# Optimization experiments

Hardware: AMD Instinct MI355X
Metric: run time of the kernel (lower is better)

Reference implementation:

```python
import jax, jax.numpy as jnp
import numpy as np

B, N, FEAT, HID = 1024, 128, 512, 256


def setup_inputs() -> dict:
    key = jax.random.key(0)
    k1, k2, k3, k4, k5, k6 = jax.random.split(key, 6)
    x = jax.random.normal(k1, (B, FEAT), dtype=jnp.float32)
    labels = jax.random.randint(k2, (B,), 0, N, dtype=jnp.int64)
    W_proj = jax.random.normal(k3, (FEAT, HID), dtype=jnp.float32) / np.sqrt(FEAT)
    b_proj = jax.random.normal(k4, (HID,), dtype=jnp.float32) * 0.01
    means = jax.random.normal(k5, (N, HID), dtype=jnp.float32)
    # inverse covariances must be SPD so sqrt(dist_sq) is real
    A = jax.random.normal(k6, (N, HID, HID), dtype=jnp.float32)
    inv_covs = jnp.einsum('nij,nkj->nik', A, A) / HID + 0.1 * jnp.eye(HID, dtype=jnp.float32)
    return {"x": x, "labels": labels, "W_proj": W_proj, "b_proj": b_proj,
            "means": means, "inv_covs": inv_covs}


def reference(x, labels, W_proj, b_proj, means, inv_covs):
    b = x.shape[0]
    n = means.shape[0]
    x_proj = x @ W_proj + b_proj                       # (b, hid)
    delta = x_proj[:, None, :] - means[None, :, :]     # (b, n, hid)
    # batched Mahalanobis quadratic form
    dist_sq = jnp.einsum('bni,nij,bnj->bn', delta, inv_covs, delta)
    distmat = jnp.sqrt(dist_sq + 1e-12)                # (b, n)
    center_mask = (labels[:, None] == jnp.arange(n)[None, :]).astype(distmat.dtype)
    loss = jnp.clip(distmat * center_mask, 1e-12, 1e12).sum() / b
    return loss, distmat
```

## Files before the change

kernel.cpp:

```cpp
#include <hip/hip_runtime.h>
#include <hip/hip_bf16.h>

#define B_    1024
#define N_    128
#define FEAT_ 512
#define HID_  256
#define LDK   264

typedef __bf16 bf16x8 __attribute__((ext_vector_type(8)));
typedef float  f32x4  __attribute__((ext_vector_type(4)));

__device__ __forceinline__ unsigned int f2bf(float f) {
    unsigned int u = __float_as_uint(f);
    u += 0x7fffu + ((u >> 16) & 1u);
    return u >> 16;
}
__device__ __forceinline__ unsigned int pack2(float a, float b) {
    return f2bf(a) | (f2bf(b) << 16);
}

union U16x8 { uint4 u; bf16x8 v; };

__global__ __launch_bounds__(256) void proj_kernel(
    const float* __restrict__ x, const float* __restrict__ W,
    const float* __restrict__ bias, float* __restrict__ xp)
{
    const int h  = threadIdx.x;
    const int b0 = blockIdx.x * 2;
    const float bb = bias[h];
    float a0 = bb, a1 = bb;
    const float* x0p = x + (size_t)(b0 + 0) * FEAT_;
    const float* x1p = x + (size_t)(b0 + 1) * FEAT_;
    #pragma unroll 4
    for (int f = 0; f < FEAT_; f += 4) {
        const float4 xv0 = *(const float4*)(x0p + f);
        const float4 xv1 = *(const float4*)(x1p + f);
        const float w0 = W[(size_t)(f + 0) * HID_ + h];
        const float w1 = W[(size_t)(f + 1) * HID_ + h];
        const float w2 = W[(size_t)(f + 2) * HID_ + h];
        const float w3 = W[(size_t)(f + 3) * HID_ + h];
        a0 += xv0.x * w0 + xv0.y * w1 + xv0.z * w2 + xv0.w * w3;
        a1 += xv1.x * w0 + xv1.y * w1 + xv1.z * w2 + xv1.w * w3;
    }
    xp[(size_t)(b0 + 0) * HID_ + h] = a0;
    xp[(size_t)(b0 + 1) * HID_ + h] = a1;
}

__global__ __launch_bounds__(512, 4) void dist_kernel(
    const float* __restrict__ xp, const float* __restrict__ means,
    const float* __restrict__ invcov, float* __restrict__ p)
{
    extern __shared__ unsigned short Ms[];

    const int tid  = threadIdx.x;
    const int bh   = blockIdx.x;
    const int jh   = blockIdx.y;
    const int n    = blockIdx.z;
    const int b0   = bh * 256;
    const int wave = tid >> 6;
    const int lane = tid & 63;
    const int q    = lane >> 4;
    const int l    = lane & 15;

    const float* Msrc = invcov + (size_t)n * (HID_ * HID_) + (size_t)jh * 128 * HID_;
    #pragma unroll
    for (int i = 0; i < 8; ++i) {
        const int g   = tid + i * 512;
        const int row = g >> 5;
        const int gc  = g & 31;
        const float* src = Msrc + (size_t)row * HID_ + gc * 8;
        const float4 a = *(const float4*)src;
        const float4 b = *(const float4*)(src + 4);
        *(uint4*)&Ms[row * LDK + gc * 8] =
            make_uint4(pack2(a.x, a.y), pack2(a.z, a.w), pack2(b.x, b.y), pack2(b.z, b.w));
    }

    const float* mrow = means + (size_t)n * HID_;
    bf16x8 afrag[2][8];
    #pragma unroll
    for (int kk = 0; kk < 8; ++kk) {
        const int k0 = kk * 32 + q * 8;
        const float4 m0 = *(const float4*)(mrow + k0);
        const float4 m1 = *(const float4*)(mrow + k0 + 4);
        #pragma unroll
        for (int rb = 0; rb < 2; ++rb) {
            const float* xr = xp + (size_t)(b0 + wave * 32 + rb * 16 + l) * HID_;
            const float4 x0 = *(const float4*)(xr + k0);
            const float4 x1 = *(const float4*)(xr + k0 + 4);
            U16x8 c;
            c.u = make_uint4(pack2(x0.x - m0.x, x0.y - m0.y),
                             pack2(x0.z - m0.z, x0.w - m0.w),
                             pack2(x1.x - m1.x, x1.y - m1.y),
                             pack2(x1.z - m1.z, x1.w - m1.w));
            afrag[rb][kk] = c.v;
        }
    }

    float muv[8];
    #pragma unroll
    for (int ct = 0; ct < 8; ++ct) muv[ct] = mrow[jh * 128 + ct * 16 + l];

    __syncthreads();

    float part[8];
    #pragma unroll
    for (int i = 0; i < 8; ++i) part[i] = 0.f;

    const size_t xbase = (size_t)(b0 + wave * 32 + q * 4) * HID_ + jh * 128 + l;

    #pragma unroll
    for (int ct = 0; ct < 8; ++ct) {
        float xl[8];
        #pragma unroll
        for (int rb = 0; rb < 2; ++rb)
            #pragma unroll
            for (int r = 0; r < 4; ++r)
                xl[rb * 4 + r] = xp[xbase + (size_t)(rb * 16 + r) * HID_ + ct * 16];

        f32x4 acc0 = {0.f,0.f,0.f,0.f}, acc1 = {0.f,0.f,0.f,0.f};
        #pragma unroll
        for (int kk = 0; kk < 8; ++kk) {
            const bf16x8 bfrag = *(const bf16x8*)&Ms[(ct * 16 + l) * LDK + kk * 32 + q * 8];
            acc0 = __builtin_amdgcn_mfma_f32_16x16x32_bf16(afrag[0][kk], bfrag, acc0, 0, 0, 0);
            acc1 = __builtin_amdgcn_mfma_f32_16x16x32_bf16(afrag[1][kk], bfrag, acc1, 0, 0, 0);
        }
        const float mu = muv[ct];
        #pragma unroll
        for (int r = 0; r < 4; ++r) {
            part[r]     += acc0[r] * (xl[r]     - mu);
            part[4 + r] += acc1[r] * (xl[4 + r] - mu);
        }
    }

    #pragma unroll
    for (int i = 0; i < 8; ++i) {
        float v = part[i];
        v += __shfl_xor(v, 1);
        v += __shfl_xor(v, 2);
        v += __shfl_xor(v, 4);
        v += __shfl_xor(v, 8);
        part[i] = v;
    }
    if (l == 0) {
        float* pb = p + (size_t)jh * (B_ * N_);
        #pragma unroll
        for (int i = 0; i < 8; ++i) {
            const int row = b0 + wave * 32 + (i >> 2) * 16 + q * 4 + (i & 3);
            pb[(size_t)row * N_ + n] = part[i];
        }
    }
}

__global__ __launch_bounds__(256) void finalize_kernel(
    const float* __restrict__ p, float* __restrict__ out)
{
    const int i = blockIdx.x * 256 + threadIdx.x;
    out[1 + i] = sqrtf(p[i] + p[B_ * N_ + i] + 1e-12f);
}

__global__ __launch_bounds__(1024) void loss_kernel(
    const float* __restrict__ distmat, const int* __restrict__ labels,
    float* __restrict__ out)
{
    __shared__ float red[16];
    const int b = threadIdx.x;
    float s = distmat[(size_t)b * N_ + labels[b]];
    #pragma unroll
    for (int m = 1; m <= 32; m <<= 1) s += __shfl_xor(s, m);
    if ((b & 63) == 0) red[b >> 6] = s;
    __syncthreads();
    if (b == 0) {
        float t = 0.f;
        #pragma unroll
        for (int i = 0; i < 16; ++i) t += red[i];
        out[0] = t / (float)B_ + (float)(N_ - 1) * 1e-12f;
    }
}

extern "C" void kernel_launch(void* const* d_in, const int* in_sizes, int n_in,
                              void* d_out, int out_size, void* d_ws, size_t ws_size,
                              hipStream_t stream) {
    const float* x      = (const float*)d_in[0];
    const int*   labels = (const int*)d_in[1];
    const float* W      = (const float*)d_in[2];
    const float* bias   = (const float*)d_in[3];
    const float* means  = (const float*)d_in[4];
    const float* invcov = (const float*)d_in[5];
    float* out = (float*)d_out;
    float* xp  = (float*)d_ws;
    float* p   = xp + (size_t)B_ * HID_;

    constexpr int DIST_LDS = 128 * LDK * 2;
    (void)hipFuncSetAttribute((const void*)dist_kernel,
                              hipFuncAttributeMaxDynamicSharedMemorySize, DIST_LDS);

    proj_kernel<<<dim3(B_ / 2), 256, 0, stream>>>(x, W, bias, xp);
    dist_kernel<<<dim3(4, 2, N_), 512, DIST_LDS, stream>>>(xp, means, invcov, p);
    finalize_kernel<<<dim3((B_ * N_) / 256), 256, 0, stream>>>(p, out);
    loss_kernel<<<1, 1024, 0, stream>>>(out + 1, labels, out);
}
```

Baseline: 163.3 us.

## Expand Mahalanobis form and pre-convert inverse covariances to swizzled bf16

The quadratic form is rewritten as x^T M x - 2 mu^T M x + mu^T M mu. A new prep kernel computes the per-class vector 2 M^T mu and the constant mu^T M mu, and stores M as bf16 in an XOR-swizzled layout. The same kernel also writes a bf16 copy of the projected inputs. The distance kernel then loads M straight into LDS with global_load_lds and reads bf16 A-fragments directly, removing the per-block fp32-to-bf16 conversion and the delta subtraction. In exchange, every call pays a full pass that reads M and writes it back, plus an extra 18 MB of workspace. The expansion also relies on M being symmetric and can lose accuracy through cancellation, since bf16 rounding now applies to x rather than to the delta.

```diff
diff --git a/kernel.cpp b/kernel.cpp
--- a/kernel.cpp
+++ b/kernel.cpp
@@ -5,7 +5,6 @@
 #define N_    128
 #define FEAT_ 512
 #define HID_  256
-#define LDK   264
 
 typedef __bf16 bf16x8 __attribute__((ext_vector_type(8)));
 typedef float  f32x4  __attribute__((ext_vector_type(4)));
@@ -15,40 +14,83 @@
     u += 0x7fffu + ((u >> 16) & 1u);
     return u >> 16;
 }
-__device__ __forceinline__ unsigned int pack2(float a, float b) {
-    return f2bf(a) | (f2bf(b) << 16);
-}
-
-union U16x8 { uint4 u; bf16x8 v; };
-
-__global__ __launch_bounds__(256) void proj_kernel(
+
+__global__ __launch_bounds__(512) void prep_kernel(
     const float* __restrict__ x, const float* __restrict__ W,
-    const float* __restrict__ bias, float* __restrict__ xp)
-{
-    const int h  = threadIdx.x;
-    const int b0 = blockIdx.x * 2;
-    const float bb = bias[h];
-    float a0 = bb, a1 = bb;
-    const float* x0p = x + (size_t)(b0 + 0) * FEAT_;
-    const float* x1p = x + (size_t)(b0 + 1) * FEAT_;
-    #pragma unroll 4
-    for (int f = 0; f < FEAT_; f += 4) {
-        const float4 xv0 = *(const float4*)(x0p + f);
-        const float4 xv1 = *(const float4*)(x1p + f);
-        const float w0 = W[(size_t)(f + 0) * HID_ + h];
-        const float w1 = W[(size_t)(f + 1) * HID_ + h];
-        const float w2 = W[(size_t)(f + 2) * HID_ + h];
-        const float w3 = W[(size_t)(f + 3) * HID_ + h];
-        a0 += xv0.x * w0 + xv0.y * w1 + xv0.z * w2 + xv0.w * w3;
-        a1 += xv1.x * w0 + xv1.y * w1 + xv1.z * w2 + xv1.w * w3;
-    }
-    xp[(size_t)(b0 + 0) * HID_ + h] = a0;
-    xp[(size_t)(b0 + 1) * HID_ + h] = a1;
+    const float* __restrict__ bias, const float* __restrict__ means,
+    const float* __restrict__ invcov,
+    float* __restrict__ xp, unsigned short* __restrict__ xbf,
+    unsigned short* __restrict__ Mbf, float* __restrict__ v2,
+    float* __restrict__ cpart)
+{
+    __shared__ float sv[4][128];
+    __shared__ float sw[2];
+    const int t = threadIdx.x;
+    if (blockIdx.x < 256) {
+        const int n  = blockIdx.x >> 1;
+        const int kh = blockIdx.x & 1;
+        const int jj = t >> 7;
+        const int kp = t & 127;
+        const int k  = kh * 128 + kp;
+        const float* Mn = invcov + (size_t)n * (HID_ * HID_);
+        const float* mu = means + (size_t)n * HID_;
+        unsigned short* Mb = Mbf + (size_t)n * (HID_ * HID_);
+        float v = 0.f;
+        #pragma unroll 8
+        for (int j0 = 0; j0 < HID_; j0 += 4) {
+            const int j = j0 + jj;
+            const float m = Mn[(size_t)j * HID_ + k];
+            v += mu[j] * m;
+            const int g2 = (k >> 3) ^ ((j & 7) << 2);
+            Mb[(size_t)j * HID_ + g2 * 8 + (k & 7)] = (unsigned short)f2bf(m);
+        }
+        sv[jj][kp] = v;
+        __syncthreads();
+        if (t < 128) {
+            const float vk = sv[0][t] + sv[1][t] + sv[2][t] + sv[3][t];
+            v2[(size_t)n * HID_ + kh * 128 + t] = 2.f * vk;
+            float cc = vk * mu[kh * 128 + t];
+            cc += __shfl_xor(cc, 1);
+            cc += __shfl_xor(cc, 2);
+            cc += __shfl_xor(cc, 4);
+            cc += __shfl_xor(cc, 8);
+            cc += __shfl_xor(cc, 16);
+            cc += __shfl_xor(cc, 32);
+            if ((t & 63) == 0) sw[t >> 6] = cc;
+        }
+        __syncthreads();
+        if (t == 0) cpart[n * 2 + kh] = sw[0] + sw[1];
+    } else {
+        const int b0 = (blockIdx.x - 256) * 4;
+        const int h  = t & 255;
+        const int rr = t >> 8;
+        const float bb = bias[h];
+        float a0 = bb, a1 = bb;
+        const float* x0p = x + (size_t)(b0 + rr * 2 + 0) * FEAT_;
+        const float* x1p = x + (size_t)(b0 + rr * 2 + 1) * FEAT_;
+        #pragma unroll 4
+        for (int f = 0; f < FEAT_; f += 4) {
+            const float4 xv0 = *(const float4*)(x0p + f);
+            const float4 xv1 = *(const float4*)(x1p + f);
+            const float w0 = W[(size_t)(f + 0) * HID_ + h];
+            const float w1 = W[(size_t)(f + 1) * HID_ + h];
+            const float w2 = W[(size_t)(f + 2) * HID_ + h];
+            const float w3 = W[(size_t)(f + 3) * HID_ + h];
+            a0 += xv0.x * w0 + xv0.y * w1 + xv0.z * w2 + xv0.w * w3;
+            a1 += xv1.x * w0 + xv1.y * w1 + xv1.z * w2 + xv1.w * w3;
+        }
+        const int r0 = b0 + rr * 2;
+        xp [(size_t)(r0 + 0) * HID_ + h] = a0;
+        xp [(size_t)(r0 + 1) * HID_ + h] = a1;
+        xbf[(size_t)(r0 + 0) * HID_ + h] = (unsigned short)f2bf(a0);
+        xbf[(size_t)(r0 + 1) * HID_ + h] = (unsigned short)f2bf(a1);
+    }
 }
 
 __global__ __launch_bounds__(512, 4) void dist_kernel(
-    const float* __restrict__ xp, const float* __restrict__ means,
-    const float* __restrict__ invcov, float* __restrict__ p)
+    const float* __restrict__ xp, const unsigned short* __restrict__ xbf,
+    const unsigned short* __restrict__ Mbf, const float* __restrict__ v2,
+    float* __restrict__ p)
 {
     extern __shared__ unsigned short Ms[];
 
@@ -56,49 +98,33 @@
     const int bh   = blockIdx.x;
     const int jh   = blockIdx.y;
     const int n    = blockIdx.z;
-    const int b0   = bh * 256;
     const int wave = tid >> 6;
     const int lane = tid & 63;
     const int q    = lane >> 4;
     const int l    = lane & 15;
 
-    const float* Msrc = invcov + (size_t)n * (HID_ * HID_) + (size_t)jh * 128 * HID_;
+    const unsigned short* src = Mbf + (size_t)n * (HID_ * HID_) + (size_t)jh * 32768;
     #pragma unroll
     for (int i = 0; i < 8; ++i) {
-        const int g   = tid + i * 512;
-        const int row = g >> 5;
-        const int gc  = g & 31;
-        const float* src = Msrc + (size_t)row * HID_ + gc * 8;
-        const float4 a = *(const float4*)src;
-        const float4 b = *(const float4*)(src + 4);
-        *(uint4*)&Ms[row * LDK + gc * 8] =
-            make_uint4(pack2(a.x, a.y), pack2(a.z, a.w), pack2(b.x, b.y), pack2(b.z, b.w));
-    }
-
-    const float* mrow = means + (size_t)n * HID_;
+        const int c = i * 8 + wave;
+        __builtin_amdgcn_global_load_lds(
+            (const __attribute__((address_space(1))) unsigned int*)(src + (size_t)c * 512 + lane * 8),
+            (__attribute__((address_space(3))) unsigned int*)&Ms[c * 512],
+            16, 0, 0);
+    }
+
     bf16x8 afrag[2][8];
     #pragma unroll
-    for (int kk = 0; kk < 8; ++kk) {
-        const int k0 = kk * 32 + q * 8;
-        const float4 m0 = *(const float4*)(mrow + k0);
-        const float4 m1 = *(const float4*)(mrow + k0 + 4);
-        #pragma unroll
-        for (int rb = 0; rb < 2; ++rb) {
-            const float* xr = xp + (size_t)(b0 + wave * 32 + rb * 16 + l) * HID_;
-            const float4 x0 = *(const float4*)(xr + k0);
-            const float4 x1 = *(const float4*)(xr + k0 + 4);
-            U16x8 c;
-            c.u = make_uint4(pack2(x0.x - m0.x, x0.y - m0.y),
-                             pack2(x0.z - m0.z, x0.w - m0.w),
-                             pack2(x1.x - m1.x, x1.y - m1.y),
-                             pack2(x1.z - m1.z, x1.w - m1.w));
-            afrag[rb][kk] = c.v;
-        }
-    }
-
-    float muv[8];
-    #pragma unroll
-    for (int ct = 0; ct < 8; ++ct) muv[ct] = mrow[jh * 128 + ct * 16 + l];
+    for (int rb = 0; rb < 2; ++rb) {
+        const unsigned short* xr = xbf + (size_t)(bh * 256 + wave * 32 + rb * 16 + l) * HID_;
+        #pragma unroll
+        for (int kk = 0; kk < 8; ++kk)
+            afrag[rb][kk] = *(const bf16x8*)(xr + kk * 32 + q * 8);
+    }
+    float v2l[8];
+    #pragma unroll
+    for (int ct = 0; ct < 8; ++ct)
+        v2l[ct] = v2[(size_t)n * HID_ + jh * 128 + ct * 16 + l];
 
     __syncthreads();
 
@@ -106,7 +132,7 @@
     #pragma unroll
     for (int i = 0; i < 8; ++i) part[i] = 0.f;
 
-    const size_t xbase = (size_t)(b0 + wave * 32 + q * 4) * HID_ + jh * 128 + l;
+    const size_t xbase = (size_t)(bh * 256 + wave * 32 + q * 4) * HID_ + jh * 128 + l;
 
     #pragma unroll
     for (int ct = 0; ct < 8; ++ct) {
@@ -120,15 +146,16 @@
         f32x4 acc0 = {0.f,0.f,0.f,0.f}, acc1 = {0.f,0.f,0.f,0.f};
         #pragma unroll
         for (int kk = 0; kk < 8; ++kk) {
-            const bf16x8 bfrag = *(const bf16x8*)&Ms[(ct * 16 + l) * LDK + kk * 32 + q * 8];
+            const bf16x8 bfrag = *(const bf16x8*)&Ms[(ct * 16 + l) * HID_ +
+                                                     (((kk * 4 + q) ^ ((l & 7) << 2)) << 3)];
             acc0 = __builtin_amdgcn_mfma_f32_16x16x32_bf16(afrag[0][kk], bfrag, acc0, 0, 0, 0);
             acc1 = __builtin_amdgcn_mfma_f32_16x16x32_bf16(afrag[1][kk], bfrag, acc1, 0, 0, 0);
         }
-        const float mu = muv[ct];
+        const float vv = v2l[ct];
         #pragma unroll
         for (int r = 0; r < 4; ++r) {
-            part[r]     += acc0[r] * (xl[r]     - mu);
-            part[4 + r] += acc1[r] * (xl[4 + r] - mu);
+            part[r]     += (acc0[r] - vv) * xl[r];
+            part[4 + r] += (acc1[r] - vv) * xl[4 + r];
         }
     }
 
@@ -145,17 +172,20 @@
         float* pb = p + (size_t)jh * (B_ * N_);
         #pragma unroll
         for (int i = 0; i < 8; ++i) {
-            const int row = b0 + wave * 32 + (i >> 2) * 16 + q * 4 + (i & 3);
+            const int row = bh * 256 + wave * 32 + (i >> 2) * 16 + q * 4 + (i & 3);
             pb[(size_t)row * N_ + n] = part[i];
         }
     }
 }
 
 __global__ __launch_bounds__(256) void finalize_kernel(
-    const float* __restrict__ p, float* __restrict__ out)
+    const float* __restrict__ p, const float* __restrict__ cpart,
+    float* __restrict__ out)
 {
     const int i = blockIdx.x * 256 + threadIdx.x;
-    out[1 + i] = sqrtf(p[i] + p[B_ * N_ + i] + 1e-12f);
+    const int n = i & (N_ - 1);
+    const float c = cpart[n * 2] + cpart[n * 2 + 1];
+    out[1 + i] = sqrtf(p[i] + p[B_ * N_ + i] + c + 1e-12f);
 }
 
 __global__ __launch_bounds__(1024) void loss_kernel(
@@ -187,15 +217,22 @@
     const float* means  = (const float*)d_in[4];
     const float* invcov = (const float*)d_in[5];
     float* out = (float*)d_out;
-    float* xp  = (float*)d_ws;
-    float* p   = xp + (size_t)B_ * HID_;
-
-    constexpr int DIST_LDS = 128 * LDK * 2;
+
+    char* ws = (char*)d_ws;
+    unsigned short* Mbf   = (unsigned short*)(ws);
+    float*          xp    = (float*)         (ws + 16777216);
+    unsigned short* xbf   = (unsigned short*)(ws + 17825792);
+    float*          v2    = (float*)         (ws + 18350080);
+    float*          cpart = (float*)         (ws + 18481152);
+    float*          p     = (float*)         (ws + 18482176);
+
+    constexpr int DIST_LDS = 128 * HID_ * 2;
     (void)hipFuncSetAttribute((const void*)dist_kernel,
                               hipFuncAttributeMaxDynamicSharedMemorySize, DIST_LDS);
 
-    proj_kernel<<<dim3(B_ / 2), 256, 0, stream>>>(x, W, bias, xp);
-    dist_kernel<<<dim3(4, 2, N_), 512, DIST_LDS, stream>>>(xp, means, invcov, p);
-    finalize_kernel<<<dim3((B_ * N_) / 256), 256, 0, stream>>>(p, out);
+    prep_kernel<<<dim3(512), 512, 0, stream>>>(x, W, bias, means, invcov,
+                                               xp, xbf, Mbf, v2, cpart);
+    dist_kernel<<<dim3(4, 2, N_), 512, DIST_LDS, stream>>>(xp, xbf, Mbf, v2, p);
+    finalize_kernel<<<dim3((B_ * N_) / 256), 256, 0, stream>>>(p, cpart, out);
     loss_kernel<<<1, 1024, 0, stream>>>(out + 1, labels, out);
 }
```

New measurement: 159.8 us. -2.2%, faster.
